# Kernel optimization log

Hardware: AMD Instinct MI355X
Metric: run time of the kernel (lower is better)

Reference implementation:

```python
import jax, jax.numpy as jnp
import numpy as np


def setup_inputs() -> dict:
    key = jax.random.key(0)
    k0, k1, k2, k3, k4 = jax.random.split(key, 5)
    B, L, D, N = 4, 2048, 768, 64
    u = jax.random.normal(k0, (B, L, D), dtype=jnp.float32)
    # A init per module: real part in [-1, -0.5), imag ~ N(0,1)
    A_real = -0.5 - 0.5 * jax.random.uniform(k1, (D, N), dtype=jnp.float32)
    A_imag = jax.random.normal(k2, (D, N), dtype=jnp.float32)
    B_mat = jax.random.normal(k3, (D, N), dtype=jnp.float32)
    C_mat = jax.random.normal(k4, (D, N), dtype=jnp.float32)
    log_delta = jnp.full((D,), np.log(0.1), dtype=jnp.float32)
    return {"u": u, "A_real": A_real, "A_imag": A_imag,
            "B_mat": B_mat, "C_mat": C_mat, "log_delta": log_delta}


def reference(u, A_real, A_imag, B_mat, C_mat, log_delta):
    # u: (B, L, D); A: (D, N) complex; B_mat, C_mat: (D, N); log_delta: (D,)
    Bsz, L, D = u.shape
    delta = jax.nn.softplus(log_delta)                      # (D,)
    A = A_real + 1j * A_imag                                # (D, N) complex
    dA = delta[:, None] * A                                 # Delta * A
    A_bar = jnp.exp(dA)                                     # ZOH: exp(dA)
    B_bar = (A_bar - 1.0) / A * B_mat                       # A^{-1}(exp(dA)-1)B
    CB = C_mat.astype(B_bar.dtype) * B_bar                  # (D, N)
    # Convolution kernel K[d, l] = Re(sum_n CB[d,n] * A_bar[d,n]^l), l = 0..L-1
    ell = jnp.arange(L, dtype=jnp.float32)
    P = jnp.exp(dA[:, :, None] * ell[None, None, :])        # (D, N, L) = A_bar^l
    K = jnp.einsum('dn,dnl->dl', CB, P).real                # (D, L)
    # Causal convolution y[b,l,d] = sum_{k<=l} K[d,k] * u[b,l-k,d] via FFT
    n_fft = 2 * L
    Uf = jnp.fft.rfft(u, n=n_fft, axis=1)                   # (B, nf, D)
    Kf = jnp.fft.rfft(K, n=n_fft, axis=1)                   # (D, nf)
    y = jnp.fft.irfft(Uf * Kf.T[None, :, :], n=n_fft, axis=1)[:, :L, :]
    return y.astype(u.dtype)
```

## Files before the change

### kernel.cpp

```cpp
#include <hip/hip_runtime.h>

#define D_DIM 768
#define N_DIM 64
#define L_DIM 2048
#define B_DIM 4
#define NT 8
#define UOFF 240
#define USTRIDE 388

typedef __attribute__((ext_vector_type(8))) short bf16x8;
typedef __attribute__((ext_vector_type(4))) float f32x4;

#define WS_NEEDED 6291456

__device__ __forceinline__ unsigned int bf16r(float f) {
    unsigned int u = __float_as_uint(f);
    return (u + 0x7fffu + ((u >> 16) & 1u)) >> 16;
}

__global__ __launch_bounds__(256) void s4_buildA(
    const float* __restrict__ A_real, const float* __restrict__ A_imag,
    const float* __restrict__ B_mat,  const float* __restrict__ C_mat,
    const float* __restrict__ log_delta, uint4* __restrict__ afrag)
{
    __shared__ float sm[4][6][N_DIM];
    __shared__ float kb[4][256];
    const int tid  = threadIdx.x;
    const int lane = tid & 63;
    const int wave = tid >> 6;
    const int d    = blockIdx.x * 4 + wave;

    {
        const int n = lane;
        float ld    = log_delta[d];
        float delta = log1pf(__expf(ld));
        float ar = A_real[d * N_DIM + n];
        float ai = A_imag[d * N_DIM + n];
        float dr = delta * ar, di = delta * ai;
        float e   = __expf(dr);
        float abr = e * __cosf(di);
        float abi = e * __sinf(di);
        float m1r = abr - 1.0f, m1i = abi;
        float inv = 1.0f / (ar * ar + ai * ai);
        float bc  = B_mat[d * N_DIM + n] * C_mat[d * N_DIM + n];
        float cbr = (m1r * ar + m1i * ai) * inv * bc;
        float cbi = (m1i * ar - m1r * ai) * inv * bc;
        float e64 = __expf(64.f * dr);
        float Mr  = e64 * __cosf(64.f * di);
        float Mi  = e64 * __sinf(64.f * di);
        sm[wave][0][n] = dr;  sm[wave][1][n] = di;
        sm[wave][2][n] = cbr; sm[wave][3][n] = cbi;
        sm[wave][4][n] = Mr;  sm[wave][5][n] = Mi;
    }
    __syncthreads();

    const float fl = (float)lane;
    float acc0 = 0.f, acc1 = 0.f, acc2 = 0.f, acc3 = 0.f;
    #pragma unroll 4
    for (int n = 0; n < N_DIM; ++n) {
        float dr  = sm[wave][0][n], di  = sm[wave][1][n];
        float cbr = sm[wave][2][n], cbi = sm[wave][3][n];
        float Mr  = sm[wave][4][n], Mi  = sm[wave][5][n];
        float e = __expf(dr * fl);
        float c = __cosf(di * fl);
        float s = __sinf(di * fl);
        float pr = e * c, pi = e * s;
        float t0r = cbr * pr - cbi * pi;
        float t0i = cbr * pi + cbi * pr;
        acc0 += t0r;
        float t1r = t0r * Mr - t0i * Mi;
        float t1i = t0r * Mi + t0i * Mr;
        acc1 += t1r;
        float t2r = t1r * Mr - t1i * Mi;
        float t2i = t1r * Mi + t1i * Mr;
        acc2 += t2r;
        float t3r = t2r * Mr - t2i * Mi;
        acc3 += t3r;
    }
    kb[wave][lane]       = acc0;
    kb[wave][64 + lane]  = acc1;
    kb[wave][128 + lane] = acc2;
    kb[wave][192 + lane] = acc3;
    __syncthreads();

    const int row = lane & 15, g = lane >> 4;
    const float* kw = kb[wave];
    #pragma unroll
    for (int tt = 0; tt < NT; ++tt) {
        unsigned int pk[4];
        #pragma unroll
        for (int p = 0; p < 4; ++p) {
            int k0 = 32 * tt + row - 8 * g - 2 * p;
            int k1 = k0 - 1;
            int c0 = min(255, max(0, k0));
            int c1 = min(255, max(0, k1));
            float v0 = (k0 >= 0 && k0 < 256) ? kw[c0] : 0.f;
            float v1 = (k1 >= 0 && k1 < 256) ? kw[c1] : 0.f;
            pk[p] = (bf16r(v1) << 16) | bf16r(v0);
        }
        afrag[((size_t)d * NT + tt) * 64 + lane] = make_uint4(pk[0], pk[1], pk[2], pk[3]);
    }
}

__global__ __launch_bounds__(256, 4) void s4_mfma_fused(
    const float* __restrict__ u, const uint4* __restrict__ afrag,
    float* __restrict__ y)
{
    __shared__ float lds[512 * 17];
    unsigned int* ubuf = (unsigned int*)lds;

    const int tid = threadIdx.x, lane = tid & 63, w = tid >> 6;
    const int dgrp = blockIdx.x, b = blockIdx.y, cp = blockIdx.z;
    const int d0 = dgrp * 16;
    const int L0 = cp * 512;

    {
        const int sub = tid >> 7;
        const int t7  = tid & 127;
        const int lp  = t7 >> 2;
        const int q   = t7 & 3;
        const bool guard = (cp == 0) || (cp == 3);
        #pragma unroll
        for (int it = 0; it < 6; ++it) {
            const int ch = it * 2 + sub;
            const int ll = ch * 64 + 2 * lp;
            const int gl = L0 - UOFF + ll;
            float4 va = {0.f, 0.f, 0.f, 0.f}, vb = {0.f, 0.f, 0.f, 0.f};
            if (!guard || (unsigned)gl < (unsigned)L_DIM)
                va = *(const float4*)(u + ((size_t)b * L_DIM + gl) * D_DIM + d0 + 4 * q);
            if (!guard || (unsigned)(gl + 1) < (unsigned)L_DIM)
                vb = *(const float4*)(u + ((size_t)b * L_DIM + gl + 1) * D_DIM + d0 + 4 * q);
            const int wb = ll >> 1;
            ubuf[(4 * q + 0) * USTRIDE + wb] = (bf16r(vb.x) << 16) | bf16r(va.x);
            ubuf[(4 * q + 1) * USTRIDE + wb] = (bf16r(vb.y) << 16) | bf16r(va.y);
            ubuf[(4 * q + 2) * USTRIDE + wb] = (bf16r(vb.z) << 16) | bf16r(va.z);
            ubuf[(4 * q + 3) * USTRIDE + wb] = (bf16r(vb.w) << 16) | bf16r(va.w);
        }
    }
    __syncthreads();

    const int c = lane & 15, g = lane >> 4;
    union AB { uint4 u4; bf16x8 v; };
    f32x4 accA[4], accB[4];
    const int w0 = UOFF / 2 + 8 * c + 4 * g;
    #pragma unroll
    for (int dd = 0; dd < 4; ++dd) {
        const int dl = w * 4 + dd;
        const uint4* arow = afrag + ((size_t)(d0 + dl) * NT) * 64 + lane;
        accA[dd] = (f32x4){0.f, 0.f, 0.f, 0.f};
        accB[dd] = (f32x4){0.f, 0.f, 0.f, 0.f};
        #pragma unroll
        for (int tt = 0; tt < NT; ++tt) {
            AB a, b0, b1;
            a.u4 = arow[tt * 64];
            const unsigned int* ur = ubuf + dl * USTRIDE + w0 - 16 * tt;
            b0.u4 = *(const uint4*)(ur);
            b1.u4 = *(const uint4*)(ur + 128);
            accA[dd] = __builtin_amdgcn_mfma_f32_16x16x32_bf16(a.v, b0.v, accA[dd], 0, 0, 0);
            accB[dd] = __builtin_amdgcn_mfma_f32_16x16x32_bf16(a.v, b1.v, accB[dd], 0, 0, 0);
        }
    }
    __syncthreads();

    #pragma unroll
    for (int dd = 0; dd < 4; ++dd) {
        const int dsw = (w * 4 + dd) ^ c;
        #pragma unroll
        for (int e = 0; e < 4; ++e) {
            int la = 16 * c + 4 * g + e;
            lds[la * 17 + dsw]         = accA[dd][e];
            lds[(la + 256) * 17 + dsw] = accB[dd][e];
        }
    }
    __syncthreads();

    const int lrow = tid >> 2;
    const int qq   = tid & 3;
    float* yb = y + ((size_t)b * L_DIM + L0) * D_DIM + d0 + 4 * qq;
    #pragma unroll
    for (int p = 0; p < 8; ++p) {
        int l  = p * 64 + lrow;
        int cs = (l >> 4) & 15;
        float4 v;
        v.x = lds[l * 17 + ((4 * qq + 0) ^ cs)];
        v.y = lds[l * 17 + ((4 * qq + 1) ^ cs)];
        v.z = lds[l * 17 + ((4 * qq + 2) ^ cs)];
        v.w = lds[l * 17 + ((4 * qq + 3) ^ cs)];
        *(float4*)(yb + (size_t)l * D_DIM) = v;
    }
}

#define T_TAPS 256
__global__ __launch_bounds__(256) void s4_kernelK_fb(
    const float* __restrict__ A_real, const float* __restrict__ A_imag,
    const float* __restrict__ B_mat,  const float* __restrict__ C_mat,
    const float* __restrict__ log_delta, float* __restrict__ Kt)
{
    __shared__ float sdr[N_DIM], sdi[N_DIM], scbr[N_DIM], scbi[N_DIM];
    const int d   = blockIdx.x;
    const int tid = threadIdx.x;
    if (tid < N_DIM) {
        const int n = tid;
        float ld    = log_delta[d];
        float delta = log1pf(__expf(ld));
        float ar = A_real[d * N_DIM + n];
        float ai = A_imag[d * N_DIM + n];
        float dr = delta * ar, di = delta * ai;
        float e   = __expf(dr);
        float abr = e * __cosf(di);
        float abi = e * __sinf(di);
        float m1r = abr - 1.0f, m1i = abi;
        float inv = 1.0f / (ar * ar + ai * ai);
        float bm  = B_mat[d * N_DIM + n];
        float cm  = C_mat[d * N_DIM + n];
        float bbr = (m1r * ar + m1i * ai) * inv * bm;
        float bbi = (m1i * ar - m1r * ai) * inv * bm;
        sdr[n] = dr;  sdi[n] = di;
        scbr[n] = cm * bbr;  scbi[n] = cm * bbi;
    }
    __syncthreads();
    const int k = tid;
    const float fk = (float)k;
    float acc = 0.f;
    #pragma unroll 8
    for (int n = 0; n < N_DIM; ++n) {
        float e = __expf(sdr[n] * fk);
        float c = __cosf(sdi[n] * fk);
        float s = __sinf(sdi[n] * fk);
        acc = fmaf(scbr[n], e * c, acc);
        acc = fmaf(-scbi[n], e * s, acc);
    }
    Kt[k * D_DIM + d] = acc;
}

template<bool GUARD>
__device__ __forceinline__ void conv_body_fb(
    const float* __restrict__ u, const float* __restrict__ Kt,
    float* __restrict__ y, float* __restrict__ lk, int xs)
{
    const int tid  = threadIdx.x;
    const int lane = tid & 63;
    const int wave = tid >> 6;
    const int d0   = blockIdx.y * 64;
    const int b    = blockIdx.z;
    const int l0   = xs * 64 + wave * 16;
    const float* ub = u + ((size_t)b * L_DIM) * D_DIM + d0 + lane;

    float acc[16], W[16];
    #pragma unroll
    for (int r = 0; r < 16; ++r) {
        acc[r] = 0.f;
        W[r]   = ub[(l0 + r) * D_DIM];
    }
    for (int kc = 0; kc < T_TAPS; kc += 64) {
        __syncthreads();
        const float4* Ks = (const float4*)(Kt + (size_t)kc * D_DIM + d0);
        float4* ls = (float4*)lk;
        #pragma unroll
        for (int i = 0; i < 4; ++i) {
            int rr = i * 16 + (tid >> 4);
            int cc = tid & 15;
            ls[rr * 16 + cc] = Ks[rr * (D_DIM / 4) + cc];
        }
        __syncthreads();
        #pragma unroll 1
        for (int kk0 = 0; kk0 < 64; kk0 += 16) {
            #pragma unroll
            for (int j = 0; j < 16; ++j) {
                const int k = kc + kk0 + j;
                float kv = lk[(kk0 + j) * 64 + lane];
                #pragma unroll
                for (int r = 0; r < 16; ++r)
                    acc[r] = fmaf(kv, W[(r - j) & 15], acc[r]);
                int lidx = l0 - k - 1;
                float nv;
                if (GUARD) nv = (lidx >= 0) ? ub[lidx * D_DIM] : 0.f;
                else       nv = ub[lidx * D_DIM];
                W[(15 - j) & 15] = nv;
            }
        }
    }
    float* yb = y + ((size_t)b * L_DIM + l0) * D_DIM + d0 + lane;
    #pragma unroll
    for (int r = 0; r < 16; ++r) yb[r * D_DIM] = acc[r];
}

__global__ __launch_bounds__(256) void s4_conv_fb(
    const float* __restrict__ u, const float* __restrict__ Kt, float* __restrict__ y)
{
    __shared__ float lk[64 * 64];
    const int lx = blockIdx.x;
    const int xs = ((lx & 7) << 2) | (lx >> 3);
    if (xs >= T_TAPS / 64) conv_body_fb<false>(u, Kt, y, lk, xs);
    else                   conv_body_fb<true >(u, Kt, y, lk, xs);
}

extern "C" void kernel_launch(void* const* d_in, const int* in_sizes, int n_in,
                              void* d_out, int out_size, void* d_ws, size_t ws_size,
                              hipStream_t stream) {
    const float* u         = (const float*)d_in[0];
    const float* A_real    = (const float*)d_in[1];
    const float* A_imag    = (const float*)d_in[2];
    const float* B_mat     = (const float*)d_in[3];
    const float* C_mat     = (const float*)d_in[4];
    const float* log_delta = (const float*)d_in[5];
    float* y = (float*)d_out;

    if (ws_size >= (size_t)WS_NEEDED) {
        uint4* afrag = (uint4*)d_ws;
        hipLaunchKernelGGL(s4_buildA, dim3(D_DIM / 4), dim3(256), 0, stream,
                           A_real, A_imag, B_mat, C_mat, log_delta, afrag);
        hipLaunchKernelGGL(s4_mfma_fused, dim3(48, B_DIM, 4), dim3(256), 0, stream,
                           u, afrag, y);
    } else {
        float* Kt = (float*)d_ws;
        hipLaunchKernelGGL(s4_kernelK_fb, dim3(D_DIM), dim3(T_TAPS), 0, stream,
                           A_real, A_imag, B_mat, C_mat, log_delta, Kt);
        hipLaunchKernelGGL(s4_conv_fb, dim3(L_DIM / 64, D_DIM / 64, B_DIM), dim3(256),
                           0, stream, u, Kt, y);
    }
}
```

Before: 101.3 us.

## Compute kernel taps one per thread and double fused-conv block width

The tap-building kernel now uses one block per channel with 256 threads, each computing one tap directly. This replaces the per-wave scheme that used a 64-step rotation recurrence. The fused MFMA convolution kernel moves to 512 threads per block, so each wave handles 2 channels instead of 4 and the load and store loops are halved. The goal is more parallelism and shorter per-thread serial chains, at the cost of more transcendental work in tap building and lower per-wave reuse of staged inputs.

```diff
diff --git a/kernel.cpp b/kernel.cpp
--- a/kernel.cpp
+++ b/kernel.cpp
@@ -23,15 +23,13 @@
     const float* __restrict__ B_mat,  const float* __restrict__ C_mat,
     const float* __restrict__ log_delta, uint4* __restrict__ afrag)
 {
-    __shared__ float sm[4][6][N_DIM];
-    __shared__ float kb[4][256];
-    const int tid  = threadIdx.x;
-    const int lane = tid & 63;
-    const int wave = tid >> 6;
-    const int d    = blockIdx.x * 4 + wave;
-
-    {
-        const int n = lane;
+    __shared__ float sdr[N_DIM], sdi[N_DIM], scbr[N_DIM], scbi[N_DIM];
+    __shared__ float kb[256];
+    const int d   = blockIdx.x;
+    const int tid = threadIdx.x;
+
+    if (tid < N_DIM) {
+        const int n = tid;
         float ld    = log_delta[d];
         float delta = log1pf(__expf(ld));
         float ar = A_real[d * N_DIM + n];
@@ -42,51 +40,35 @@
         float abi = e * __sinf(di);
         float m1r = abr - 1.0f, m1i = abi;
         float inv = 1.0f / (ar * ar + ai * ai);
-        float bc  = B_mat[d * N_DIM + n] * C_mat[d * N_DIM + n];
-        float cbr = (m1r * ar + m1i * ai) * inv * bc;
-        float cbi = (m1i * ar - m1r * ai) * inv * bc;
-        float e64 = __expf(64.f * dr);
-        float Mr  = e64 * __cosf(64.f * di);
-        float Mi  = e64 * __sinf(64.f * di);
-        sm[wave][0][n] = dr;  sm[wave][1][n] = di;
-        sm[wave][2][n] = cbr; sm[wave][3][n] = cbi;
-        sm[wave][4][n] = Mr;  sm[wave][5][n] = Mi;
-    }
-    __syncthreads();
-
-    const float fl = (float)lane;
-    float acc0 = 0.f, acc1 = 0.f, acc2 = 0.f, acc3 = 0.f;
-    #pragma unroll 4
-    for (int n = 0; n < N_DIM; ++n) {
-        float dr  = sm[wave][0][n], di  = sm[wave][1][n];
-        float cbr = sm[wave][2][n], cbi = sm[wave][3][n];
-        float Mr  = sm[wave][4][n], Mi  = sm[wave][5][n];
-        float e = __expf(dr * fl);
-        float c = __cosf(di * fl);
-        float s = __sinf(di * fl);
-        float pr = e * c, pi = e * s;
-        float t0r = cbr * pr - cbi * pi;
-        float t0i = cbr * pi + cbi * pr;
-        acc0 += t0r;
-        float t1r = t0r * Mr - t0i * Mi;
-        float t1i = t0r * Mi + t0i * Mr;
-        acc1 += t1r;
-        float t2r = t1r * Mr - t1i * Mi;
-        float t2i = t1r * Mi + t1i * Mr;
-        acc2 += t2r;
-        float t3r = t2r * Mr - t2i * Mi;
-        acc3 += t3r;
-    }
-    kb[wave][lane]       = acc0;
-    kb[wave][64 + lane]  = acc1;
-    kb[wave][128 + lane] = acc2;
-    kb[wave][192 + lane] = acc3;
-    __syncthreads();
-
+        float bm  = B_mat[d * N_DIM + n];
+        float cm  = C_mat[d * N_DIM + n];
+        float bbr = (m1r * ar + m1i * ai) * inv * bm;
+        float bbi = (m1i * ar - m1r * ai) * inv * bm;
+        sdr[n] = dr;  sdi[n] = di;
+        scbr[n] = cm * bbr;  scbi[n] = cm * bbi;
+    }
+    __syncthreads();
+
+    {
+        const float fk = (float)tid;
+        float acc = 0.f;
+        #pragma unroll 8
+        for (int n = 0; n < N_DIM; ++n) {
+            float e = __expf(sdr[n] * fk);
+            float c = __cosf(sdi[n] * fk);
+            float s = __sinf(sdi[n] * fk);
+            acc = fmaf(scbr[n], e * c, acc);
+            acc = fmaf(-scbi[n], e * s, acc);
+        }
+        kb[tid] = acc;
+    }
+    __syncthreads();
+
+    const int lane = tid & 63, w = tid >> 6;
     const int row = lane & 15, g = lane >> 4;
-    const float* kw = kb[wave];
-    #pragma unroll
-    for (int tt = 0; tt < NT; ++tt) {
+    #pragma unroll
+    for (int i = 0; i < 2; ++i) {
+        const int tt = w * 2 + i;
         unsigned int pk[4];
         #pragma unroll
         for (int p = 0; p < 4; ++p) {
@@ -94,15 +76,15 @@
             int k1 = k0 - 1;
             int c0 = min(255, max(0, k0));
             int c1 = min(255, max(0, k1));
-            float v0 = (k0 >= 0 && k0 < 256) ? kw[c0] : 0.f;
-            float v1 = (k1 >= 0 && k1 < 256) ? kw[c1] : 0.f;
+            float v0 = (k0 >= 0 && k0 < 256) ? kb[c0] : 0.f;
+            float v1 = (k1 >= 0 && k1 < 256) ? kb[c1] : 0.f;
             pk[p] = (bf16r(v1) << 16) | bf16r(v0);
         }
         afrag[((size_t)d * NT + tt) * 64 + lane] = make_uint4(pk[0], pk[1], pk[2], pk[3]);
     }
 }
 
-__global__ __launch_bounds__(256, 4) void s4_mfma_fused(
+__global__ __launch_bounds__(512, 4) void s4_mfma_fused(
     const float* __restrict__ u, const uint4* __restrict__ afrag,
     float* __restrict__ y)
 {
@@ -115,15 +97,12 @@
     const int L0 = cp * 512;
 
     {
-        const int sub = tid >> 7;
-        const int t7  = tid & 127;
-        const int lp  = t7 >> 2;
-        const int q   = t7 & 3;
+        const int q  = tid & 3;
+        const int lp = tid >> 2;
         const bool guard = (cp == 0) || (cp == 3);
         #pragma unroll
-        for (int it = 0; it < 6; ++it) {
-            const int ch = it * 2 + sub;
-            const int ll = ch * 64 + 2 * lp;
+        for (int it = 0; it < 3; ++it) {
+            const int ll = (it * 128 + lp) * 2;
             const int gl = L0 - UOFF + ll;
             float4 va = {0.f, 0.f, 0.f, 0.f}, vb = {0.f, 0.f, 0.f, 0.f};
             if (!guard || (unsigned)gl < (unsigned)L_DIM)
@@ -141,11 +120,11 @@
 
     const int c = lane & 15, g = lane >> 4;
     union AB { uint4 u4; bf16x8 v; };
-    f32x4 accA[4], accB[4];
+    f32x4 accA[2], accB[2];
     const int w0 = UOFF / 2 + 8 * c + 4 * g;
     #pragma unroll
-    for (int dd = 0; dd < 4; ++dd) {
-        const int dl = w * 4 + dd;
+    for (int dd = 0; dd < 2; ++dd) {
+        const int dl = w * 2 + dd;
         const uint4* arow = afrag + ((size_t)(d0 + dl) * NT) * 64 + lane;
         accA[dd] = (f32x4){0.f, 0.f, 0.f, 0.f};
         accB[dd] = (f32x4){0.f, 0.f, 0.f, 0.f};
@@ -163,8 +142,9 @@
     __syncthreads();
 
     #pragma unroll
-    for (int dd = 0; dd < 4; ++dd) {
-        const int dsw = (w * 4 + dd) ^ c;
+    for (int dd = 0; dd < 2; ++dd) {
+        const int dl  = w * 2 + dd;
+        const int dsw = dl ^ c;
         #pragma unroll
         for (int e = 0; e < 4; ++e) {
             int la = 16 * c + 4 * g + e;
@@ -178,8 +158,8 @@
     const int qq   = tid & 3;
     float* yb = y + ((size_t)b * L_DIM + L0) * D_DIM + d0 + 4 * qq;
     #pragma unroll
-    for (int p = 0; p < 8; ++p) {
-        int l  = p * 64 + lrow;
+    for (int p = 0; p < 4; ++p) {
+        int l  = p * 128 + lrow;
         int cs = (l >> 4) & 15;
         float4 v;
         v.x = lds[l * 17 + ((4 * qq + 0) ^ cs)];
@@ -308,9 +288,9 @@
 
     if (ws_size >= (size_t)WS_NEEDED) {
         uint4* afrag = (uint4*)d_ws;
-        hipLaunchKernelGGL(s4_buildA, dim3(D_DIM / 4), dim3(256), 0, stream,
+        hipLaunchKernelGGL(s4_buildA, dim3(D_DIM), dim3(256), 0, stream,
                            A_real, A_imag, B_mat, C_mat, log_delta, afrag);
-        hipLaunchKernelGGL(s4_mfma_fused, dim3(48, B_DIM, 4), dim3(256), 0, stream,
+        hipLaunchKernelGGL(s4_mfma_fused, dim3(48, B_DIM, 4), dim3(512), 0, stream,
                            u, afrag, y);
     } else {
         float* Kt = (float*)d_ws;
```

Result: no change. 101.0 us (-0.3%).
